# Kernel tuning notes

Measured on AMD Instinct MI355X. Metric: run time of the kernel, lower is better.

## Reference

```python
import jax, jax.numpy as jnp
import numpy as np

SENS = 200
DM = 128
NMAPS = 2
NLAYERS = 2
TH = 0.01
EPS = 1e-5
BATCH = 8
SEQ = 96
HEADS = 8


def setup_inputs() -> dict:
    key = jax.random.key(0)
    ks = jax.random.split(key, 8)
    x = jax.random.normal(ks[0], (BATCH, SENS, SEQ, DM), jnp.float32)
    attn_s = jax.random.uniform(ks[1], (1, BATCH, HEADS, SENS, SENS), jnp.float32)
    supports = jax.random.uniform(ks[2], (SENS, SENS), jnp.float32)
    W_conv = jax.random.normal(ks[3], (NMAPS, NLAYERS, DM, DM), jnp.float32) * 0.05
    b_conv = jnp.zeros((NMAPS, NLAYERS, DM), jnp.float32)
    bn_gamma = jnp.ones((NMAPS, DM), jnp.float32)
    bn_beta = jnp.zeros((NMAPS, DM), jnp.float32)
    W_out = jax.random.normal(ks[4], (NMAPS * DM, DM), jnp.float32) * 0.05
    b_out = jnp.zeros((DM,), jnp.float32)
    return dict(x=x, attn_s=attn_s, supports=supports, W_conv=W_conv,
                b_conv=b_conv, bn_gamma=bn_gamma, bn_beta=bn_beta,
                W_out=W_out, b_out=b_out)


def _process_map(A):
    # make_symmetric: lower triangle + mirrored strict lower triangle
    A = jnp.tril(A) + jnp.tril(A, -1).T
    # clamp: threshold on absolute value; note original returns |A| thresholded
    Aa = jnp.abs(A)
    A = jnp.where(Aa > TH, Aa, jnp.zeros_like(Aa))
    # SparseTensor.from_dense(A).t()
    return A.T


def _gcn_norm(adj_t):
    # GCNConv default: add self-loops (weight 1), symmetric D^-1/2 A D^-1/2
    A = adj_t + jnp.eye(adj_t.shape[0], dtype=adj_t.dtype)
    deg = A.sum(axis=1)
    d = jnp.where(deg > 0, jax.lax.rsqrt(deg), jnp.zeros_like(deg))
    return d[:, None] * A * d[None, :]


def reference(x, attn_s, supports, W_conv, b_conv, bn_gamma, bn_beta, W_out, b_out):
    B, N, S, D = x.shape
    # reshape_mat: [B,N,S,D] -> [B*S, N, D]
    xr = x.transpose(0, 2, 1, 3).reshape(B * S, N, D)

    # supports: [data map, adaptive map from attention (mean over batch, heads)]
    maps = [_process_map(supports), _process_map(attn_s[0].mean(axis=(0, 1)))]

    gcn_outputs = []
    for i in range(NMAPS):
        An = _gcn_norm(maps[i])  # [N,N]
        h = jnp.zeros_like(xr[..., :1]) * 0.0  # placeholder replaced below
        h = None
        for l in range(NLAYERS):
            xw = jnp.einsum('bnf,fg->bng', xr, W_conv[i, l])
            hl = jnp.einsum('mn,bng->bmg', An, xw) + b_conv[i, l]
            h = hl if h is None else h + hl
        # BatchNorm1d over feature channel (training-mode batch stats, biased var)
        mu = h.mean(axis=(0, 1))
        var = h.var(axis=(0, 1))
        hn = (h - mu) * jax.lax.rsqrt(var + EPS) * bn_gamma[i] + bn_beta[i]
        gcn_outputs.append(jax.nn.relu(hn))

    cat = jnp.concatenate(gcn_outputs, axis=-1)  # [B*S, N, NMAPS*DM]
    y = jax.nn.relu(jnp.einsum('bnc,cd->bnd', cat, W_out) + b_out)
    # inverse_reshape_mat: [B*S, N, D] -> [B, N, S, D]
    return y.reshape(B, S, N, D).transpose(0, 2, 1, 3)
```

## Files before the change

kernel.cpp:

```cpp
#include <hip/hip_runtime.h>

#define SENS 200
#define DM 128
#define SEQ 96
#define NB 8
#define BS 768
#define NTOT 153600
#define TH 0.01f
#define BN_EPS 1e-5f
#define MPAD 224
#define KP 208
#define XWS 212
#define ASROW 68

typedef __attribute__((ext_vector_type(8)))  __bf16 bf16x8;
typedef __attribute__((ext_vector_type(4)))  __bf16 bf16x4;
typedef __attribute__((ext_vector_type(16))) float  f32x16;

__device__ __forceinline__ f32x16 mfma32(bf16x8 a, bf16x8 b, f32x16 c) {
    return __builtin_amdgcn_mfma_f32_32x32x16_bf16(a, b, c, 0, 0, 0);
}
__device__ __forceinline__ bf16x8 join8(bf16x4 a, bf16x4 b) {
    bf16x8 r;
    #pragma unroll
    for (int j = 0; j < 4; ++j) { r[j] = a[j]; r[j + 4] = b[j]; }
    return r;
}

__global__ void attn_mean_kernel(const float* __restrict__ attn, float* __restrict__ mapA) {
    int idx = blockIdx.x * 256 + threadIdx.x;
    if (idx >= SENS * SENS) return;
    float s = 0.f;
    #pragma unroll 8
    for (int q = 0; q < 64; ++q) s += attn[(size_t)q * SENS * SENS + idx];
    mapA[idx] = s * (1.0f / 64.0f);
}

__global__ void build_map_kernel(const float* __restrict__ supports, const float* __restrict__ mapA,
                                 float* __restrict__ M, float* __restrict__ deg) {
    __shared__ float red[256];
    int m = blockIdx.x, map = blockIdx.y, j = threadIdx.x;
    const float* src = (map == 0) ? supports : mapA;
    float v = 0.f;
    if (j < SENS) {
        float sym = (m >= j) ? src[m * SENS + j] : src[j * SENS + m];
        float a = fabsf(sym);
        v = (a > TH) ? a : 0.f;
        M[(size_t)map * SENS * SENS + m * SENS + j] = v;
    }
    red[j] = v;
    __syncthreads();
    for (int off = 128; off > 0; off >>= 1) {
        if (j < off) red[j] += red[j + off];
        __syncthreads();
    }
    if (j == 0) deg[map * SENS + m] = red[0] + 1.0f;
}

__global__ __launch_bounds__(256) void prep2_kernel(
    const float* __restrict__ M, const float* __restrict__ deg,
    const float* __restrict__ W_conv, const float* __restrict__ b_conv,
    const float* __restrict__ W_out,
    __bf16* __restrict__ Anb, __bf16* __restrict__ Wt, __bf16* __restrict__ Wot,
    float* __restrict__ bsum, float* __restrict__ bnacc)
{
    const int bid = blockIdx.x, t = threadIdx.x;
    if (bid < 2 * MPAD) {
        const int map = bid / MPAD, m = bid % MPAD;
        const int j = t;
        if (j < KP) {
            float val = 0.f;
            if (m < SENS && j < SENS) {
                float a = M[((size_t)map * SENS + m) * SENS + j] + ((m == j) ? 1.f : 0.f);
                val = rsqrtf(deg[map * SENS + m]) * a * rsqrtf(deg[map * SENS + j]);
            }
            Anb[(((size_t)map * 13 + (j >> 4)) * MPAD + m) * 16 + (j & 15)] = (__bf16)val;
        }
    } else {
        const int idx = (bid - 2 * MPAD) * 256 + t;
        if (idx < 32768) {
            const int map = idx >> 14, g = (idx >> 7) & 127, f = idx & 127;
            const float* wp = W_conv + (size_t)map * 2 * DM * DM + f * DM + g;
            Wt[(((size_t)map * 8 + (f >> 4)) * DM + g) * 16 + (f & 15)] = (__bf16)(wp[0] + wp[DM * DM]);
        } else if (idx < 65536) {
            const int k = idx - 32768, d = k >> 8, c = k & 255;
            Wot[(((size_t)(c >> 4)) * DM + d) * 16 + (c & 15)] = (__bf16)W_out[c * DM + d];
        } else if (idx < 65792) {
            const int k = idx - 65536, map = k >> 7, g = k & 127;
            bsum[k] = b_conv[(map * 2) * DM + g] + b_conv[(map * 2 + 1) * DM + g];
        } else if (idx < 66304) {
            bnacc[idx - 65792] = 0.f;
        }
    }
}

__global__ __launch_bounds__(448, 6) void conv_kernel(
    const float* __restrict__ x, const __bf16* __restrict__ Anb,
    const __bf16* __restrict__ Wt, const float* __restrict__ bsum,
    __bf16* __restrict__ h, float* __restrict__ bnacc)
{
    __shared__ __bf16 xw[64 * XWS];
    const int bx = blockIdx.x;
    const int bs = bx >> 2, map = (bx >> 1) & 1, gh = bx & 1;
    const int b = bs / SEQ, s = bs % SEQ;
    const int t = threadIdx.x, w = t >> 6, lane = t & 63;
    const int l31 = lane & 31, hi = lane >> 5;

    {
        f32x16 acc[2];
        #pragma unroll
        for (int p = 0; p < 2; ++p)
            #pragma unroll
            for (int r = 0; r < 16; ++r) acc[p][r] = 0.f;
        const int n = w * 32 + l31;
        const bool valid = (n < SENS);
        const float* xrow = x + (((size_t)b * SENS + (valid ? n : 0)) * SEQ + s) * DM + hi * 8;
        const __bf16* wb = Wt + (((size_t)map * 8) * DM + gh * 64 + l31) * 16 + hi * 8;
        #pragma unroll
        for (int kc = 0; kc < 8; ++kc) {
            float4 v0 = *(const float4*)(xrow + kc * 16);
            float4 v1 = *(const float4*)(xrow + kc * 16 + 4);
            bf16x8 bfrag;
            bfrag[0] = (__bf16)v0.x; bfrag[1] = (__bf16)v0.y;
            bfrag[2] = (__bf16)v0.z; bfrag[3] = (__bf16)v0.w;
            bfrag[4] = (__bf16)v1.x; bfrag[5] = (__bf16)v1.y;
            bfrag[6] = (__bf16)v1.z; bfrag[7] = (__bf16)v1.w;
            if (!valid) {
                #pragma unroll
                for (int j = 0; j < 8; ++j) bfrag[j] = (__bf16)0.f;
            }
            const __bf16* wp = wb + (size_t)kc * DM * 16;
            acc[0] = mfma32(*(const bf16x8*)wp, bfrag, acc[0]);
            acc[1] = mfma32(*(const bf16x8*)(wp + 32 * 16), bfrag, acc[1]);
        }
        if (n < KP) {
            #pragma unroll
            for (int p = 0; p < 2; ++p)
                #pragma unroll
                for (int r = 0; r < 16; ++r) {
                    const int g = p * 32 + (r & 3) + 8 * (r >> 2) + 4 * hi;
                    xw[g * XWS + n] = (__bf16)acc[p][r];
                }
        }
    }
    __syncthreads();

    f32x16 acc2[2];
    #pragma unroll
    for (int p = 0; p < 2; ++p)
        #pragma unroll
        for (int r = 0; r < 16; ++r) acc2[p][r] = 0.f;
    {
        const __bf16* ab = Anb + (((size_t)map * 13) * MPAD + w * 32 + l31) * 16 + hi * 8;
        #pragma unroll
        for (int kc = 0; kc < 13; ++kc) {
            bf16x8 afrag = *(const bf16x8*)(ab + (size_t)kc * MPAD * 16);
            #pragma unroll
            for (int p = 0; p < 2; ++p) {
                bf16x8 bfrag = *(const bf16x8*)(xw + (p * 32 + l31) * XWS + kc * 16 + hi * 8);
                acc2[p] = mfma32(afrag, bfrag, acc2[p]);
            }
        }
    }
    float bsn[2], bsq[2];
    #pragma unroll
    for (int p = 0; p < 2; ++p) {
        const float bias = bsum[map * DM + gh * 64 + p * 32 + l31];
        bf16x8 h0, h1;
        float s2 = 0.f, q = 0.f;
        #pragma unroll
        for (int r = 0; r < 16; ++r) {
            const float v = acc2[p][r] + bias;
            if (r < 8) h0[r] = (__bf16)v; else h1[r - 8] = (__bf16)v;
            const int m = w * 32 + (r & 3) + 8 * (r >> 2) + 4 * hi;
            if (m < SENS) { s2 += v; q += v * v; }
        }
        __bf16* hp = h + ((((size_t)(bs * 2 + map) * 7 + w) * 4 + (gh * 2 + p)) * 64 + lane) * 16;
        *(bf16x8*)hp = h0;
        *(bf16x8*)(hp + 8) = h1;
        s2 += __shfl_xor(s2, 32);
        q += __shfl_xor(q, 32);
        bsn[p] = s2; bsq[p] = q;
    }
    __syncthreads();
    float* red = (float*)xw;
    if (hi == 0) {
        #pragma unroll
        for (int p = 0; p < 2; ++p) {
            red[(p * 32 + l31) * 7 + w] = bsn[p];
            red[(64 + p * 32 + l31) * 7 + w] = bsq[p];
        }
    }
    __syncthreads();
    if (t < 128) {
        const int sq = t >> 6, g = t & 63;
        float s2 = 0.f;
        #pragma unroll
        for (int k = 0; k < 7; ++k) s2 += red[(sq * 64 + g) * 7 + k];
        atomicAdd(&bnacc[sq * 256 + map * DM + gh * 64 + g], s2);
    }
}

__device__ __forceinline__ void out_stage(int cn, int t, int bs,
                                          const __bf16* __restrict__ h,
                                          const float* sc_s, const float* sh_s,
                                          __bf16* dst)
{
    const int mapn = cn >> 1;
    const __bf16* hb = h + ((size_t)(bs * 2 + mapn) * 28 + (cn & 1) * 2) * 1024;
    bf16x8 vv[4];
    #pragma unroll
    for (int it = 0; it < 4; ++it) {
        const int idx = it * 512 + t;
        if (idx < 1792)
            vv[it] = *(const bf16x8*)(hb + ((size_t)(idx >> 8) * 4 + ((idx >> 7) & 1)) * 1024
                                          + ((idx >> 1) & 63) * 16 + (idx & 1) * 8);
    }
    #pragma unroll
    for (int it = 0; it < 4; ++it) {
        const int idx = it * 512 + t;
        if (idx < 1792) {
            const int half = idx & 1, lane_s = (idx >> 1) & 63;
            const int ctl = (idx >> 7) & 1, strip = idx >> 8;
            const int cl = ctl * 32 + (lane_s & 31);
            const int cg = mapn * DM + (cn & 1) * 64 + cl;
            const float scv = sc_s[cg], shv = sh_s[cg];
            const int mbase = strip * 32 + 4 * (lane_s >> 5) + 16 * half;
            #pragma unroll
            for (int q2 = 0; q2 < 8; ++q2) {
                const int row = mbase + (q2 & 3) + 8 * (q2 >> 2);
                const float fv = (float)vv[it][q2] * scv + shv;
                dst[row * ASROW + cl] = (__bf16)fmaxf(fv, 0.f);
            }
        }
    }
}

__global__ __launch_bounds__(512) void out_kernel(
    const __bf16* __restrict__ h, const __bf16* __restrict__ Wot,
    const float* __restrict__ bnacc,
    const float* __restrict__ gamma, const float* __restrict__ beta,
    const float* __restrict__ b_out, float* __restrict__ out)
{
    __shared__ __bf16 As[2][MPAD * ASROW];
    __shared__ float sc_s[256], sh_s[256];
    const int bs = blockIdx.x;
    const int b = bs / SEQ, s = bs % SEQ;
    const int t = threadIdx.x, w = t >> 6, lane = t & 63;
    const int l31 = lane & 31, hi = lane >> 5;
    const int dct = w & 3, sbase = w >> 2;
    if (t < 256) {
        const float mu = bnacc[t] * (1.f / (float)NTOT);
        const float var = bnacc[256 + t] * (1.f / (float)NTOT) - mu * mu;
        const float sc = gamma[t] * rsqrtf(var + BN_EPS);
        sc_s[t] = sc;
        sh_s[t] = beta[t] - mu * sc;
    }
    f32x16 acc[4];
    {
        const float bo = b_out[dct * 32 + l31];
        #pragma unroll
        for (int i = 0; i < 4; ++i)
            #pragma unroll
            for (int r = 0; r < 16; ++r) acc[i][r] = bo;
    }
    __syncthreads();
    out_stage(0, t, bs, h, sc_s, sh_s, &As[0][0]);
    __syncthreads();
    for (int c = 0; c < 4; ++c) {
        #pragma unroll
        for (int kc = 0; kc < 4; ++kc) {
            bf16x8 bfrag = *(const bf16x8*)(Wot + ((size_t)(c * 4 + kc) * DM + dct * 32 + l31) * 16 + hi * 8);
            #pragma unroll
            for (int i = 0; i < 4; ++i) {
                const int strip = sbase + 2 * i;
                if (strip >= 7) break;
                const __bf16* ap = &As[c & 1][(strip * 32 + l31) * ASROW + kc * 16 + hi * 8];
                acc[i] = mfma32(join8(*(const bf16x4*)ap, *(const bf16x4*)(ap + 4)), bfrag, acc[i]);
            }
        }
        if (c < 3) out_stage(c + 1, t, bs, h, sc_s, sh_s, &As[(c + 1) & 1][0]);
        __syncthreads();
    }
    #pragma unroll
    for (int i = 0; i < 4; ++i) {
        const int strip = sbase + 2 * i;
        if (strip >= 7) break;
        #pragma unroll
        for (int r = 0; r < 16; ++r) {
            const int m = strip * 32 + (r & 3) + 8 * (r >> 2) + 4 * hi;
            if (m < SENS)
                out[(((size_t)b * SENS + m) * SEQ + s) * DM + dct * 32 + l31] = fmaxf(acc[i][r], 0.f);
        }
    }
}

extern "C" void kernel_launch(void* const* d_in, const int* in_sizes, int n_in,
                              void* d_out, int out_size, void* d_ws, size_t ws_size,
                              hipStream_t stream) {
    const float* x        = (const float*)d_in[0];
    const float* attn     = (const float*)d_in[1];
    const float* supports = (const float*)d_in[2];
    const float* W_conv   = (const float*)d_in[3];
    const float* b_conv   = (const float*)d_in[4];
    const float* gamma    = (const float*)d_in[5];
    const float* beta     = (const float*)d_in[6];
    const float* W_out    = (const float*)d_in[7];
    const float* b_out    = (const float*)d_in[8];
    float* out = (float*)d_out;
    char* base = (char*)d_ws;

    float*  mapA  = (float*)(base + 0);
    float*  Mbuf  = (float*)(base + 160000);
    float*  deg   = (float*)(base + 480000);
    float*  bnacc = (float*)(base + 481664);
    float*  bsum  = (float*)(base + 483712);
    __bf16* Wt    = (__bf16*)(base + 484736);
    __bf16* Wot   = (__bf16*)(base + 550272);
    __bf16* Anb   = (__bf16*)(base + 615808);
    __bf16* h     = (__bf16*)(base + 1048576);

    attn_mean_kernel<<<157, 256, 0, stream>>>(attn, mapA);
    build_map_kernel<<<dim3(SENS, 2), 256, 0, stream>>>(supports, mapA, Mbuf, deg);
    prep2_kernel<<<2 * MPAD + 260, 256, 0, stream>>>(Mbuf, deg, W_conv, b_conv, W_out,
                                                     Anb, Wt, Wot, bsum, bnacc);
    conv_kernel<<<BS * 4, 448, 0, stream>>>(x, Anb, Wt, bsum, h, bnacc);
    out_kernel<<<BS, 512, 0, stream>>>(h, Wot, bnacc, gamma, beta, b_out, out);
}
```

Measured before the change: 274.4 us.

## Merge conv blocks so each block handles both maps and all feature columns

Before this change, each (batch,seq) slice was split across four blocks (two maps times two feature halves), so every block re-read the same x rows from global memory. Now one block covers the whole slice: it loops over both maps and computes all 128 output features. x is loaded once per map per block, and the atomic adds for the BN statistics are combined into fewer, larger batches. The cost is a bigger shared-memory tile, more accumulator registers, a lower occupancy hint, and a grid of only 768 blocks, which may underfill the GPU.

```diff
diff --git a/kernel.cpp b/kernel.cpp
--- a/kernel.cpp
+++ b/kernel.cpp
@@ -94,110 +94,118 @@
     }
 }
 
-__global__ __launch_bounds__(448, 6) void conv_kernel(
+__global__ __launch_bounds__(448, 4) void conv_kernel(
     const float* __restrict__ x, const __bf16* __restrict__ Anb,
     const __bf16* __restrict__ Wt, const float* __restrict__ bsum,
     __bf16* __restrict__ h, float* __restrict__ bnacc)
 {
-    __shared__ __bf16 xw[64 * XWS];
-    const int bx = blockIdx.x;
-    const int bs = bx >> 2, map = (bx >> 1) & 1, gh = bx & 1;
+    __shared__ __bf16 xw[128 * XWS];
+    const int bs = blockIdx.x;
     const int b = bs / SEQ, s = bs % SEQ;
     const int t = threadIdx.x, w = t >> 6, lane = t & 63;
     const int l31 = lane & 31, hi = lane >> 5;
 
-    {
-        f32x16 acc[2];
-        #pragma unroll
-        for (int p = 0; p < 2; ++p)
-            #pragma unroll
-            for (int r = 0; r < 16; ++r) acc[p][r] = 0.f;
-        const int n = w * 32 + l31;
-        const bool valid = (n < SENS);
-        const float* xrow = x + (((size_t)b * SENS + (valid ? n : 0)) * SEQ + s) * DM + hi * 8;
-        const __bf16* wb = Wt + (((size_t)map * 8) * DM + gh * 64 + l31) * 16 + hi * 8;
-        #pragma unroll
-        for (int kc = 0; kc < 8; ++kc) {
-            float4 v0 = *(const float4*)(xrow + kc * 16);
-            float4 v1 = *(const float4*)(xrow + kc * 16 + 4);
-            bf16x8 bfrag;
-            bfrag[0] = (__bf16)v0.x; bfrag[1] = (__bf16)v0.y;
-            bfrag[2] = (__bf16)v0.z; bfrag[3] = (__bf16)v0.w;
-            bfrag[4] = (__bf16)v1.x; bfrag[5] = (__bf16)v1.y;
-            bfrag[6] = (__bf16)v1.z; bfrag[7] = (__bf16)v1.w;
-            if (!valid) {
+    const int n = w * 32 + l31;
+    const bool valid = (n < SENS);
+    const float* xrow = x + (((size_t)b * SENS + (valid ? n : 0)) * SEQ + s) * DM + hi * 8;
+
+    float bsn[2][4], bsq[2][4];
+
+    #pragma unroll 1
+    for (int map = 0; map < 2; ++map) {
+        if (map) __syncthreads();
+        {
+            f32x16 acc[4];
+            #pragma unroll
+            for (int gt = 0; gt < 4; ++gt)
                 #pragma unroll
-                for (int j = 0; j < 8; ++j) bfrag[j] = (__bf16)0.f;
-            }
-            const __bf16* wp = wb + (size_t)kc * DM * 16;
-            acc[0] = mfma32(*(const bf16x8*)wp, bfrag, acc[0]);
-            acc[1] = mfma32(*(const bf16x8*)(wp + 32 * 16), bfrag, acc[1]);
-        }
-        if (n < KP) {
-            #pragma unroll
-            for (int p = 0; p < 2; ++p)
+                for (int r = 0; r < 16; ++r) acc[gt][r] = 0.f;
+            const __bf16* wb = Wt + (((size_t)map * 8) * DM + l31) * 16 + hi * 8;
+            #pragma unroll
+            for (int kc = 0; kc < 8; ++kc) {
+                float4 v0 = *(const float4*)(xrow + kc * 16);
+                float4 v1 = *(const float4*)(xrow + kc * 16 + 4);
+                bf16x8 bfrag;
+                bfrag[0] = (__bf16)v0.x; bfrag[1] = (__bf16)v0.y;
+                bfrag[2] = (__bf16)v0.z; bfrag[3] = (__bf16)v0.w;
+                bfrag[4] = (__bf16)v1.x; bfrag[5] = (__bf16)v1.y;
+                bfrag[6] = (__bf16)v1.z; bfrag[7] = (__bf16)v1.w;
+                if (!valid) {
+                    #pragma unroll
+                    for (int j = 0; j < 8; ++j) bfrag[j] = (__bf16)0.f;
+                }
+                const __bf16* wp = wb + (size_t)kc * DM * 16;
                 #pragma unroll
-                for (int r = 0; r < 16; ++r) {
-                    const int g = p * 32 + (r & 3) + 8 * (r >> 2) + 4 * hi;
-                    xw[g * XWS + n] = (__bf16)acc[p][r];
+                for (int gt = 0; gt < 4; ++gt)
+                    acc[gt] = mfma32(*(const bf16x8*)(wp + gt * 32 * 16), bfrag, acc[gt]);
+            }
+            if (n < KP) {
+                #pragma unroll
+                for (int gt = 0; gt < 4; ++gt)
+                    #pragma unroll
+                    for (int r = 0; r < 16; ++r) {
+                        const int g = gt * 32 + (r & 3) + 8 * (r >> 2) + 4 * hi;
+                        xw[g * XWS + n] = (__bf16)acc[gt][r];
+                    }
+            }
+        }
+        __syncthreads();
+
+        f32x16 acc2[4];
+        #pragma unroll
+        for (int gt = 0; gt < 4; ++gt)
+            #pragma unroll
+            for (int r = 0; r < 16; ++r) acc2[gt][r] = 0.f;
+        {
+            const __bf16* ab = Anb + (((size_t)map * 13) * MPAD + w * 32 + l31) * 16 + hi * 8;
+            #pragma unroll 2
+            for (int kc = 0; kc < 13; ++kc) {
+                bf16x8 afrag = *(const bf16x8*)(ab + (size_t)kc * MPAD * 16);
+                #pragma unroll
+                for (int gt = 0; gt < 4; ++gt) {
+                    bf16x8 bfrag = *(const bf16x8*)(xw + (gt * 32 + l31) * XWS + kc * 16 + hi * 8);
+                    acc2[gt] = mfma32(afrag, bfrag, acc2[gt]);
                 }
-        }
-    }
-    __syncthreads();
-
-    f32x16 acc2[2];
-    #pragma unroll
-    for (int p = 0; p < 2; ++p)
-        #pragma unroll
-        for (int r = 0; r < 16; ++r) acc2[p][r] = 0.f;
-    {
-        const __bf16* ab = Anb + (((size_t)map * 13) * MPAD + w * 32 + l31) * 16 + hi * 8;
-        #pragma unroll
-        for (int kc = 0; kc < 13; ++kc) {
-            bf16x8 afrag = *(const bf16x8*)(ab + (size_t)kc * MPAD * 16);
-            #pragma unroll
-            for (int p = 0; p < 2; ++p) {
-                bf16x8 bfrag = *(const bf16x8*)(xw + (p * 32 + l31) * XWS + kc * 16 + hi * 8);
-                acc2[p] = mfma32(afrag, bfrag, acc2[p]);
-            }
-        }
-    }
-    float bsn[2], bsq[2];
-    #pragma unroll
-    for (int p = 0; p < 2; ++p) {
-        const float bias = bsum[map * DM + gh * 64 + p * 32 + l31];
-        bf16x8 h0, h1;
-        float s2 = 0.f, q = 0.f;
-        #pragma unroll
-        for (int r = 0; r < 16; ++r) {
-            const float v = acc2[p][r] + bias;
-            if (r < 8) h0[r] = (__bf16)v; else h1[r - 8] = (__bf16)v;
-            const int m = w * 32 + (r & 3) + 8 * (r >> 2) + 4 * hi;
-            if (m < SENS) { s2 += v; q += v * v; }
-        }
-        __bf16* hp = h + ((((size_t)(bs * 2 + map) * 7 + w) * 4 + (gh * 2 + p)) * 64 + lane) * 16;
-        *(bf16x8*)hp = h0;
-        *(bf16x8*)(hp + 8) = h1;
-        s2 += __shfl_xor(s2, 32);
-        q += __shfl_xor(q, 32);
-        bsn[p] = s2; bsq[p] = q;
+            }
+        }
+        #pragma unroll
+        for (int gt = 0; gt < 4; ++gt) {
+            const float bias = bsum[map * DM + gt * 32 + l31];
+            bf16x8 h0, h1;
+            float s2 = 0.f, q = 0.f;
+            #pragma unroll
+            for (int r = 0; r < 16; ++r) {
+                const float v = acc2[gt][r] + bias;
+                if (r < 8) h0[r] = (__bf16)v; else h1[r - 8] = (__bf16)v;
+                const int m = w * 32 + (r & 3) + 8 * (r >> 2) + 4 * hi;
+                if (m < SENS) { s2 += v; q += v * v; }
+            }
+            __bf16* hp = h + ((((size_t)(bs * 2 + map) * 7 + w) * 4 + gt) * 64 + lane) * 16;
+            *(bf16x8*)hp = h0;
+            *(bf16x8*)(hp + 8) = h1;
+            s2 += __shfl_xor(s2, 32);
+            q += __shfl_xor(q, 32);
+            bsn[map][gt] = s2; bsq[map][gt] = q;
+        }
     }
     __syncthreads();
     float* red = (float*)xw;
     if (hi == 0) {
         #pragma unroll
-        for (int p = 0; p < 2; ++p) {
-            red[(p * 32 + l31) * 7 + w] = bsn[p];
-            red[(64 + p * 32 + l31) * 7 + w] = bsq[p];
-        }
-    }
-    __syncthreads();
-    if (t < 128) {
-        const int sq = t >> 6, g = t & 63;
+        for (int map = 0; map < 2; ++map)
+            #pragma unroll
+            for (int gt = 0; gt < 4; ++gt) {
+                red[(((map * 2 + 0) * 128) + gt * 32 + l31) * 7 + w] = bsn[map][gt];
+                red[(((map * 2 + 1) * 128) + gt * 32 + l31) * 7 + w] = bsq[map][gt];
+            }
+    }
+    __syncthreads();
+    for (int i = t; i < 512; i += 448) {
+        const int map = i >> 8, sq = (i >> 7) & 1, g = i & 127;
         float s2 = 0.f;
         #pragma unroll
-        for (int k = 0; k < 7; ++k) s2 += red[(sq * 64 + g) * 7 + k];
-        atomicAdd(&bnacc[sq * 256 + map * DM + gh * 64 + g], s2);
+        for (int k = 0; k < 7; ++k) s2 += red[i * 7 + k];
+        atomicAdd(&bnacc[sq * 256 + map * DM + g], s2);
     }
 }
 
@@ -324,6 +332,6 @@
     build_map_kernel<<<dim3(SENS, 2), 256, 0, stream>>>(supports, mapA, Mbuf, deg);
     prep2_kernel<<<2 * MPAD + 260, 256, 0, stream>>>(Mbuf, deg, W_conv, b_conv, W_out,
                                                      Anb, Wt, Wot, bsum, bnacc);
-    conv_kernel<<<BS * 4, 448, 0, stream>>>(x, Anb, Wt, bsum, h, bnacc);
+    conv_kernel<<<BS, 448, 0, stream>>>(x, Anb, Wt, bsum, h, bnacc);
     out_kernel<<<BS, 512, 0, stream>>>(h, Wot, bnacc, gamma, beta, b_out, out);
 }
```

Result: faster. 261.3 us (-4.8%).
